# Kernel optimization log

Hardware: AMD Instinct MI355X
Metric: run time of the kernel (lower is better)

The kernel has to match this reference:

```python
import jax, jax.numpy as jnp
import numpy as np

N_EMBD = 768
N_HEAD = 12
HEAD_DIM = N_EMBD // N_HEAD
EPS = 1e-6


def setup_inputs() -> dict:
    key = jax.random.key(0)
    ks = jax.random.split(key, 8)
    B, T, C = 4, 2048, N_EMBD
    s = 0.02
    return {
        "x": jax.random.normal(ks[0], (B, T, C), jnp.float32),
        "ln1_w": jnp.ones((C,), jnp.float32),
        "ln1_b": jnp.zeros((C,), jnp.float32),
        "W_attn": jax.random.normal(ks[1], (C, 3 * C), jnp.float32) * s,
        "b_attn": jnp.zeros((3 * C,), jnp.float32),
        "W_attn_proj": jax.random.normal(ks[2], (C, C), jnp.float32) * s,
        "b_attn_proj": jnp.zeros((C,), jnp.float32),
        "ln2_w": jnp.ones((C,), jnp.float32),
        "ln2_b": jnp.zeros((C,), jnp.float32),
        "W_fc": jax.random.normal(ks[3], (C, 4 * C), jnp.float32) * s,
        "b_fc": jnp.zeros((4 * C,), jnp.float32),
        "W_mlp_proj": jax.random.normal(ks[4], (4 * C, C), jnp.float32) * s,
        "b_mlp_proj": jnp.zeros((C,), jnp.float32),
    }


def layer_norm(x, w, b):
    # Faithful to MyLayerNorm: (x - mean) / (std + eps), std with ddof=0
    mean = jnp.mean(x, axis=-1, keepdims=True)
    std = jnp.sqrt(jnp.mean((x - mean) ** 2, axis=-1, keepdims=True))
    return w * (x - mean) / (std + EPS) + b


def attention(h, W_attn, b_attn, W_proj, b_proj):
    B, T, C = h.shape
    qkv = h @ W_attn + b_attn                      # [B,T,3C]
    q, k, v = jnp.split(qkv, 3, axis=-1)
    # [B,T,C] -> [B,H,T,D]
    def to_heads(t):
        return t.reshape(B, T, N_HEAD, HEAD_DIM).transpose(0, 2, 1, 3)
    q, k, v = to_heads(q), to_heads(k), to_heads(v)
    att = jnp.einsum("bhtd,bhsd->bhts", q, k) * (1.0 / np.sqrt(HEAD_DIM))
    causal = jnp.tril(jnp.ones((T, T), bool))[None, None]
    att = jnp.where(causal, att, -jnp.inf)
    att = jax.nn.softmax(att, axis=-1)
    y = jnp.einsum("bhts,bhsd->bhtd", att, v)      # [B,H,T,D]
    y = y.transpose(0, 2, 1, 3).reshape(B, T, C)
    return y @ W_proj + b_proj


def mlp(h, W_fc, b_fc, W_proj, b_proj):
    h = jax.nn.gelu(h @ W_fc + b_fc, approximate=False)
    return h @ W_proj + b_proj


def reference(x, ln1_w, ln1_b, W_attn, b_attn, W_attn_proj, b_attn_proj,
              ln2_w, ln2_b, W_fc, b_fc, W_mlp_proj, b_mlp_proj):
    x = x + attention(layer_norm(x, ln1_w, ln1_b), W_attn, b_attn, W_attn_proj, b_attn_proj)
    x = x + mlp(layer_norm(x, ln2_w, ln2_b), W_fc, b_fc, W_mlp_proj, b_mlp_proj)
    return x
```

## Files before the change

### kernel.cpp

```cpp
#include <hip/hip_runtime.h>
#include <hip/hip_bf16.h>
#include <math.h>

#define N_EMBD 768
#define N_HEAD 12
#define HEAD_DIM 64
#define TOKENS 8192
#define SEQ 2048
#define BATCH 4
#define NQT (SEQ / 64)

typedef __attribute__((ext_vector_type(8))) short short8;
typedef __attribute__((ext_vector_type(4))) short short4v;
typedef __attribute__((ext_vector_type(4))) float f32x4;

__device__ __forceinline__ short f2bf(float f) {
    unsigned u = __builtin_bit_cast(unsigned, f);
    unsigned r = (u + 0x7fffu + ((u >> 16) & 1u)) >> 16;
    return (short)r;
}
__device__ __forceinline__ short f2bf_fast(float f) {
    unsigned u = __builtin_bit_cast(unsigned, f);
    return (short)((u + 0x8000u) >> 16);
}

__device__ __forceinline__ float exp2_raw(float x) {
#if __has_builtin(__builtin_amdgcn_exp2f)
    return __builtin_amdgcn_exp2f(x);
#else
    return exp2f(x);
#endif
}

__device__ __forceinline__ float gelu_fast(float x) {
    float z = 1.5957691216057308f * x * (1.0f + 0.044715f * x * x);
    return x / (1.0f + __expf(-z));
}

__device__ __forceinline__ void gld16(const void* g, void* l) {
    __builtin_amdgcn_global_load_lds(
        (const __attribute__((address_space(1))) unsigned int*)g,
        (__attribute__((address_space(3))) unsigned int*)l, 16, 0, 0);
}

__global__ __launch_bounds__(256) void wT_all(
        const float* __restrict__ Wa, short* __restrict__ Ta,
        const float* __restrict__ Wp, short* __restrict__ Tp,
        const float* __restrict__ Wf, short* __restrict__ Tf,
        const float* __restrict__ Wm, short* __restrict__ Tm) {
    __shared__ float T[32][33];
    int id = blockIdx.x;
    const float* W; short* Wt; int K, N;
    if (id < 1728)      { W = Wa; Wt = Ta; K = 768;  N = 2304; }
    else if (id < 2304) { W = Wp; Wt = Tp; K = 768;  N = 768;  id -= 1728; }
    else if (id < 4608) { W = Wf; Wt = Tf; K = 768;  N = 3072; id -= 2304; }
    else                { W = Wm; Wt = Tm; K = 3072; N = 768;  id -= 4608; }
    int tn = N >> 5;
    int n0 = (id % tn) * 32, k0 = (id / tn) * 32;
    int c = threadIdx.x & 31, r0 = threadIdx.x >> 5;
#pragma unroll
    for (int i = 0; i < 32; i += 8)
        T[r0 + i][c] = W[(size_t)(k0 + r0 + i) * N + n0 + c];
    __syncthreads();
#pragma unroll
    for (int i = 0; i < 32; i += 8)
        Wt[(size_t)(n0 + r0 + i) * K + k0 + c] = f2bf(T[c][r0 + i]);
}

__global__ __launch_bounds__(256) void ln_bf_kernel(const float* __restrict__ x,
                                                    const float* __restrict__ w,
                                                    const float* __restrict__ b,
                                                    short* __restrict__ out) {
    int row = blockIdx.x * 4 + (threadIdx.x >> 6);
    int lane = threadIdx.x & 63;
    const float4* xr = (const float4*)(x + (size_t)row * N_EMBD);
    const float4* wr = (const float4*)w;
    const float4* br = (const float4*)b;

    float4 v[3];
#pragma unroll
    for (int i = 0; i < 3; ++i) v[i] = xr[lane + 64 * i];
    float s = 0.f;
#pragma unroll
    for (int i = 0; i < 3; ++i) s += v[i].x + v[i].y + v[i].z + v[i].w;
#pragma unroll
    for (int off = 1; off < 64; off <<= 1) s += __shfl_xor(s, off, 64);
    float mean = s * (1.f / 768.f);

    float var = 0.f;
#pragma unroll
    for (int i = 0; i < 3; ++i) {
        float a0 = v[i].x - mean, a1 = v[i].y - mean,
              a2 = v[i].z - mean, a3 = v[i].w - mean;
        var += a0 * a0 + a1 * a1 + a2 * a2 + a3 * a3;
    }
#pragma unroll
    for (int off = 1; off < 64; off <<= 1) var += __shfl_xor(var, off, 64);
    float inv = 1.f / (sqrtf(var * (1.f / 768.f)) + 1e-6f);

    short4v* yr = (short4v*)(out + (size_t)row * N_EMBD);
#pragma unroll
    for (int i = 0; i < 3; ++i) {
        float4 wv = wr[lane + 64 * i], bv = br[lane + 64 * i];
        short4v o;
        o[0] = f2bf(wv.x * (v[i].x - mean) * inv + bv.x);
        o[1] = f2bf(wv.y * (v[i].y - mean) * inv + bv.y);
        o[2] = f2bf(wv.z * (v[i].z - mean) * inv + bv.z);
        o[3] = f2bf(wv.w * (v[i].w - mean) * inv + bv.w);
        yr[lane + 64 * i] = o;
    }
}

template <int ACT, int VOUT, int SWAP>
__global__ __launch_bounds__(256) void gemm_mfma(
        const short* __restrict__ A,
        const short* __restrict__ Bt,
        const float* __restrict__ bias,
        short* __restrict__ outp,
        short* __restrict__ vt,
        int M, int N, int K) {
    __shared__ short As[8192];
    __shared__ short Bs[8192];
    int tid = threadIdx.x;
    int wave = tid >> 6, lane = tid & 63;
    int quad = lane >> 4, l15 = lane & 15;
    int m0 = blockIdx.x * 128, n0 = blockIdx.y * 128;
    int wm = wave >> 1, wn = wave & 1;
    int sr = lane >> 2, sc = (lane & 3) * 8;

    f32x4 acc[4][4];
#pragma unroll
    for (int i = 0; i < 4; ++i)
#pragma unroll
        for (int j = 0; j < 4; ++j) acc[i][j] = (f32x4){0.f, 0.f, 0.f, 0.f};

    const short* ag = A + (size_t)(m0 + wave * 32 + sr) * K + sc;
    const short* bg = Bt + (size_t)(n0 + wave * 32 + sr) * K + sc;
    int woff = wave * 1024;

    gld16(ag, &As[woff]);
    gld16(ag + (size_t)16 * K, &As[woff + 512]);
    gld16(bg, &Bs[woff]);
    gld16(bg + (size_t)16 * K, &Bs[woff + 512]);

    int nk = K >> 5;
    for (int it = 0; it < nk; ++it) {
        int cb = (it & 1) * 4096;
        __syncthreads();
        if (it + 1 < nk) {
            int nb = ((it + 1) & 1) * 4096 + woff;
            int kn = (it + 1) << 5;
            gld16(ag + kn, &As[nb]);
            gld16(ag + kn + (size_t)16 * K, &As[nb + 512]);
            gld16(bg + kn, &Bs[nb]);
            gld16(bg + kn + (size_t)16 * K, &Bs[nb + 512]);
        }
        short8 af[4], bfr[4];
#pragma unroll
        for (int mt = 0; mt < 4; ++mt)
            af[mt] = *(const short8*)&As[cb + (wm * 64 + mt * 16 + l15) * 32 + quad * 8];
#pragma unroll
        for (int nt = 0; nt < 4; ++nt)
            bfr[nt] = *(const short8*)&Bs[cb + (wn * 64 + nt * 16 + l15) * 32 + quad * 8];
#pragma unroll
        for (int mt = 0; mt < 4; ++mt)
#pragma unroll
            for (int nt = 0; nt < 4; ++nt) {
                if (SWAP)
                    acc[mt][nt] = __builtin_amdgcn_mfma_f32_16x16x32_bf16(
                        bfr[nt], af[mt], acc[mt][nt], 0, 0, 0);
                else
                    acc[mt][nt] = __builtin_amdgcn_mfma_f32_16x16x32_bf16(
                        af[mt], bfr[nt], acc[mt][nt], 0, 0, 0);
            }
    }

    if (SWAP) {
#pragma unroll
        for (int nt = 0; nt < 4; ++nt) {
            int colb = n0 + wn * 64 + nt * 16 + quad * 4;
            f32x4 b4 = *(const f32x4*)&bias[colb];
#pragma unroll
            for (int mt = 0; mt < 4; ++mt) {
                int row = m0 + wm * 64 + mt * 16 + l15;
                short4v o4;
#pragma unroll
                for (int r = 0; r < 4; ++r) {
                    float v = acc[mt][nt][r] + b4[r];
                    if (ACT) v = gelu_fast(v);
                    o4[r] = f2bf(v);
                }
                *(short4v*)&outp[(size_t)row * N + colb] = o4;
            }
        }
        return;
    }

    if (VOUT && n0 >= 1536) {
#pragma unroll
        for (int mt = 0; mt < 4; ++mt) {
            int row0 = m0 + wm * 64 + mt * 16 + quad * 4;
            int b = row0 >> 11, t0 = row0 & 2047;
#pragma unroll
            for (int nt = 0; nt < 4; ++nt) {
                int col = n0 + wn * 64 + nt * 16 + l15;
                int vcol = col - 1536;
                int bh = b * N_HEAD + (vcol >> 6);
                int d = vcol & 63;
                float bi = bias[col];
                short4v o;
#pragma unroll
                for (int r = 0; r < 4; ++r) o[r] = f2bf(acc[mt][nt][r] + bi);
                *(short4v*)&vt[((size_t)bh * 64 + d) * SEQ + t0] = o;
            }
        }
        return;
    }

#pragma unroll
    for (int mt = 0; mt < 4; ++mt) {
        int row0 = m0 + wm * 64 + mt * 16 + quad * 4;
#pragma unroll
        for (int nt = 0; nt < 4; ++nt) {
            int col = n0 + wn * 64 + nt * 16 + l15;
            float bi = bias[col];
#pragma unroll
            for (int r = 0; r < 4; ++r) {
                float v = acc[mt][nt][r] + bi;
                if (ACT) v = gelu_fast(v);
                outp[(size_t)(row0 + r) * N + col] = f2bf(v);
            }
        }
    }
}

__global__ __launch_bounds__(256) void gemm_mfma_n64(
        const short* __restrict__ A,
        const short* __restrict__ Bt,
        const float* __restrict__ bias,
        const float* __restrict__ res,
        float* __restrict__ outp,
        int M, int N, int K) {
    __shared__ short As[16384];
    __shared__ short Bs[8192];
    int tid = threadIdx.x;
    int wave = tid >> 6, lane = tid & 63;
    int quad = lane >> 4, l15 = lane & 15;
    int m0 = blockIdx.x * 128, n0 = blockIdx.y * 64;
    int wm = wave >> 1, wn = wave & 1;
    int sr = lane >> 2, sc = (lane & 3) * 8;

    f32x4 acc[4][2];
#pragma unroll
    for (int i = 0; i < 4; ++i)
#pragma unroll
        for (int j = 0; j < 2; ++j) acc[i][j] = (f32x4){0.f, 0.f, 0.f, 0.f};

    const short* gptr[6];
    int loff[6];
    bool isa[6];
#pragma unroll
    for (int j = 0; j < 6; ++j) {
        int c = wave * 6 + j;
        if (c < 16) {
            int ks = c >> 3, r0 = (c & 7) * 16;
            gptr[j] = A + (size_t)(m0 + r0 + sr) * K + ks * 32 + sc;
            loff[j] = ks * 4096 + r0 * 32; isa[j] = true;
        } else {
            int cb = c - 16;
            int ks = cb >> 2, r0 = (cb & 3) * 16;
            gptr[j] = Bt + (size_t)(n0 + r0 + sr) * K + ks * 32 + sc;
            loff[j] = ks * 2048 + r0 * 32; isa[j] = false;
        }
    }
    int nk = K >> 6;

    auto stage = [&](int t) {
        int ba = (t & 1) << 13, bb = (t & 1) << 12;
        int kn = t << 6;
#pragma unroll
        for (int j = 0; j < 6; ++j)
            gld16(gptr[j] + kn, isa[j] ? &As[ba + loff[j]] : &Bs[bb + loff[j]]);
    };

    stage(0);

    for (int it = 0; it < nk; ++it) {
        int cba = (it & 1) << 13, cbb = (it & 1) << 12;
        __syncthreads();
        if (it + 1 < nk) stage(it + 1);
#pragma unroll
        for (int ks = 0; ks < 2; ++ks) {
            short8 af[4], bfr[2];
#pragma unroll
            for (int mt = 0; mt < 4; ++mt)
                af[mt] = *(const short8*)&As[cba + ks * 4096 +
                                             (wm * 64 + mt * 16 + l15) * 32 + quad * 8];
#pragma unroll
            for (int nt = 0; nt < 2; ++nt)
                bfr[nt] = *(const short8*)&Bs[cbb + ks * 2048 +
                                              (wn * 32 + nt * 16 + l15) * 32 + quad * 8];
#pragma unroll
            for (int mt = 0; mt < 4; ++mt)
#pragma unroll
                for (int nt = 0; nt < 2; ++nt)
                    acc[mt][nt] = __builtin_amdgcn_mfma_f32_16x16x32_bf16(
                        bfr[nt], af[mt], acc[mt][nt], 0, 0, 0);
        }
    }

#pragma unroll
    for (int nt = 0; nt < 2; ++nt) {
        int colb = n0 + wn * 32 + nt * 16 + quad * 4;
        f32x4 b4 = *(const f32x4*)&bias[colb];
#pragma unroll
        for (int mt = 0; mt < 4; ++mt) {
            int row = m0 + wm * 64 + mt * 16 + l15;
            f32x4 rv = *(const f32x4*)&res[(size_t)row * N + colb];
            f32x4 ov;
#pragma unroll
            for (int r = 0; r < 4; ++r) ov[r] = acc[mt][nt][r] + b4[r] + rv[r];
            *(f32x4*)&outp[(size_t)row * N + colb] = ov;
        }
    }
}

template <bool DIAG>
__device__ __forceinline__ void attn_kt(
        const short* __restrict__ Ks, const short* __restrict__ Vs,
        short* __restrict__ Ps, int cb,
        const short8* qf, short8 ones,
        f32x4* o, f32x4& lacc,
        int wave, int quad, int l15, int pswz) {
    f32x4 sacc[4];
#pragma unroll
    for (int nt = 0; nt < 4; ++nt) sacc[nt] = (f32x4){0.f, 0.f, 0.f, 0.f};
#pragma unroll
    for (int nt = 0; nt < 4; ++nt)
#pragma unroll
        for (int ks = 0; ks < 2; ++ks) {
            short8 kf = *(const short8*)&Ks[cb + ks * 2048 + (nt * 16 + l15) * 32 + quad * 8];
            sacc[nt] = __builtin_amdgcn_mfma_f32_16x16x32_bf16(qf[ks], kf, sacc[nt], 0, 0, 0);
        }

#pragma unroll
    for (int nt = 0; nt < 4; ++nt) {
        int scol = nt * 16 + l15;
        int base = (scol >> 5) * 2048 + (scol & 31);
#pragma unroll
        for (int r = 0; r < 4; ++r) {
            float p = exp2_raw(fmaf(sacc[nt][r], 0.18033688011112042f,
                                    -5.770780163555854f));
            if (DIAG && (scol > wave * 16 + quad * 4 + r)) p = 0.f;
            Ps[(base + (wave * 16 + quad * 4 + r) * 32) ^ (quad << 4)] = f2bf_fast(p);
        }
    }

    short8 pf0 = *(const short8*)&Ps[((wave * 16 + l15) * 32 + quad * 8) ^ pswz];
    short8 pf1 = *(const short8*)&Ps[(2048 + (wave * 16 + l15) * 32 + quad * 8) ^ pswz];
    lacc = __builtin_amdgcn_mfma_f32_16x16x32_bf16(pf0, ones, lacc, 0, 0, 0);
    lacc = __builtin_amdgcn_mfma_f32_16x16x32_bf16(pf1, ones, lacc, 0, 0, 0);
#pragma unroll
    for (int nt = 0; nt < 4; ++nt) {
        short8 vf0 = *(const short8*)&Vs[cb + (nt * 16 + l15) * 32 + quad * 8];
        short8 vf1 = *(const short8*)&Vs[cb + 2048 + (nt * 16 + l15) * 32 + quad * 8];
        o[nt] = __builtin_amdgcn_mfma_f32_16x16x32_bf16(pf0, vf0, o[nt], 0, 0, 0);
        o[nt] = __builtin_amdgcn_mfma_f32_16x16x32_bf16(pf1, vf1, o[nt], 0, 0, 0);
    }
}

__device__ __forceinline__ void attn_tile(
        const short* __restrict__ qkv, const short* __restrict__ Vt,
        short* __restrict__ y, int bh, int qt,
        short* Ks, short* Vs, short* Ps) {
    int tid = threadIdx.x;
    int wave = tid >> 6, lane = tid & 63;
    int quad = lane >> 4, l15 = lane & 15;
    int h = bh % N_HEAD, b = bh / N_HEAD;
    size_t bT = (size_t)b * SEQ;
    int q0 = qt * 64;
    int sr = lane >> 2, sc = (lane & 3) * 8;

    const short ONE_BF = (short)0x3F80;
    short8 ones;
#pragma unroll
    for (int j = 0; j < 8; ++j) ones[j] = ONE_BF;

    const short* qrow = qkv + (bT + q0 + wave * 16 + l15) * 2304 + h * 64 + quad * 8;
    short8 qf[2];
    qf[0] = *(const short8*)qrow;
    qf[1] = *(const short8*)(qrow + 32);

    const short* gp[4];
    int lo[4], adv[4];
#pragma unroll
    for (int j = 0; j < 4; ++j) {
        int c = wave * 4 + j;
        if (c < 8) {
            int sub = c >> 2, r0 = (c & 3) * 16;
            gp[j] = qkv + (bT + r0 + sr) * 2304 + 768 + h * 64 + sub * 32 + sc;
            lo[j] = sub * 2048 + r0 * 32;
            adv[j] = 64 * 2304;
        } else {
            int cv = c - 8;
            int sub = cv >> 2, r0 = (cv & 3) * 16;
            gp[j] = Vt + ((size_t)bh * 64 + r0 + sr) * SEQ + sub * 32 + sc;
            lo[j] = sub * 2048 + r0 * 32;
            adv[j] = 64;
        }
    }

    __syncthreads();
#pragma unroll
    for (int j = 0; j < 4; ++j)
        gld16(gp[j], (wave * 4 + j < 8) ? &Ks[lo[j]] : &Vs[lo[j]]);
#pragma unroll
    for (int j = 0; j < 4; ++j) gp[j] += adv[j];
    __syncthreads();

    f32x4 o[4];
#pragma unroll
    for (int nt = 0; nt < 4; ++nt) o[nt] = (f32x4){0.f, 0.f, 0.f, 0.f};
    f32x4 lacc = (f32x4){0.f, 0.f, 0.f, 0.f};

    const int pswz = ((l15 >> 2) & 3) << 4;

    for (int kt = 0; kt < qt; ++kt) {
        int cb = (kt & 1) * 4096;
        if (kt) __syncthreads();
        int nb = ((kt + 1) & 1) * 4096;
#pragma unroll
        for (int j = 0; j < 4; ++j) {
            gld16(gp[j], (wave * 4 + j < 8) ? &Ks[nb + lo[j]] : &Vs[nb + lo[j]]);
            gp[j] += adv[j];
        }
        attn_kt<false>(Ks, Vs, Ps, cb, qf, ones, o, lacc, wave, quad, l15, pswz);
    }

    if (qt) __syncthreads();
    attn_kt<true>(Ks, Vs, Ps, (qt & 1) * 4096, qf, ones, o, lacc,
                  wave, quad, l15, pswz);

    float inv[4];
#pragma unroll
    for (int r = 0; r < 4; ++r) inv[r] = 1.f / lacc[r];
#pragma unroll
    for (int nt = 0; nt < 4; ++nt)
#pragma unroll
        for (int r = 0; r < 4; ++r)
            y[(bT + q0 + wave * 16 + quad * 4 + r) * N_EMBD + h * 64 + nt * 16 + l15] =
                f2bf(o[nt][r] * inv[r]);
}

__global__ __launch_bounds__(256, 4) void attn_mfma(
        const short* __restrict__ qkv, const short* __restrict__ Vt,
        short* __restrict__ y) {
    __shared__ short Ks[8192], Vs[8192], Ps[4096];
    int bh = blockIdx.x;
    int pair = blockIdx.y;
    attn_tile(qkv, Vt, y, bh, pair, Ks, Vs, Ps);
    attn_tile(qkv, Vt, y, bh, NQT - 1 - pair, Ks, Vs, Ps);
}

extern "C" void kernel_launch(void* const* d_in, const int* in_sizes, int n_in,
                              void* d_out, int out_size, void* d_ws, size_t ws_size,
                              hipStream_t stream) {
    const float* x         = (const float*)d_in[0];
    const float* ln1_w     = (const float*)d_in[1];
    const float* ln1_b     = (const float*)d_in[2];
    const float* W_attn    = (const float*)d_in[3];
    const float* b_attn    = (const float*)d_in[4];
    const float* W_attn_pr = (const float*)d_in[5];
    const float* b_attn_pr = (const float*)d_in[6];
    const float* ln2_w     = (const float*)d_in[7];
    const float* ln2_b     = (const float*)d_in[8];
    const float* W_fc      = (const float*)d_in[9];
    const float* b_fc      = (const float*)d_in[10];
    const float* W_mlp_pr  = (const float*)d_in[11];
    const float* b_mlp_pr  = (const float*)d_in[12];
    float* out = (float*)d_out;

    const int M = TOKENS, C = N_EMBD;
    char* ws = (char*)d_ws;
    size_t region0 = (size_t)M * 3072 * 2;
    short* qkv_bf = (short*)ws;
    short* fc_bf  = (short*)ws;
    size_t off = region0;
    short* VtB   = (short*)(ws + off); off += (size_t)48 * 64 * SEQ * 2;
    short* yb    = (short*)(ws + off); off += (size_t)M * C * 2;
    short* lnb   = (short*)(ws + off); off += (size_t)M * C * 2;
    float* x1    = (float*)(ws + off); off += (size_t)M * C * 4;
    short* WaT   = (short*)(ws + off); off += (size_t)2304 * 768 * 2;
    short* WpT   = (short*)(ws + off); off += (size_t)768 * 768 * 2;
    short* WfT   = (short*)(ws + off); off += (size_t)3072 * 768 * 2;
    short* WmT   = (short*)(ws + off); off += (size_t)768 * 3072 * 2;

    wT_all<<<6912, 256, 0, stream>>>(W_attn, WaT, W_attn_pr, WpT,
                                     W_fc, WfT, W_mlp_pr, WmT);

    ln_bf_kernel<<<M / 4, 256, 0, stream>>>(x, ln1_w, ln1_b, lnb);

    gemm_mfma<0, 1, 0><<<dim3(M / 128, 2304 / 128), 256, 0, stream>>>(
        lnb, WaT, b_attn, qkv_bf, VtB, M, 2304, 768);

    attn_mfma<<<dim3(BATCH * N_HEAD, NQT / 2), 256, 0, stream>>>(qkv_bf, VtB, yb);

    gemm_mfma_n64<<<dim3(M / 128, 768 / 64), 256, 0, stream>>>(
        yb, WpT, b_attn_pr, x, x1, M, 768, 768);

    ln_bf_kernel<<<M / 4, 256, 0, stream>>>(x1, ln2_w, ln2_b, lnb);

    gemm_mfma<1, 0, 1><<<dim3(M / 128, 3072 / 128), 256, 0, stream>>>(
        lnb, WfT, b_fc, fc_bf, nullptr, M, 3072, 768);

    gemm_mfma_n64<<<dim3(M / 128, 768 / 64), 256, 0, stream>>>(
        fc_bf, WmT, b_mlp_pr, x1, out, M, 768, 3072);
}
```

Baseline: 371.5 us.

## Deepen GEMM K-tile to 64 and share K/V tiles across paired query tiles

The GEMM kernel now stages a 64-wide K slice per iteration, doubling shared memory per buffer, which halves the number of barriers and loop iterations. The attention kernel now processes its two paired query tiles (pair and NQT-1-pair) in a single pass over the key/value tiles, so the shared K/V tiles for the short tile are loaded once instead of twice. The cost is more registers for two sets of accumulators and more LDS in the GEMM (64KB), which may reduce occupancy.

```diff
diff --git a/kernel.cpp b/kernel.cpp
--- a/kernel.cpp
+++ b/kernel.cpp
@@ -119,8 +119,8 @@
         short* __restrict__ outp,
         short* __restrict__ vt,
         int M, int N, int K) {
-    __shared__ short As[8192];
-    __shared__ short Bs[8192];
+    __shared__ short As[16384];
+    __shared__ short Bs[16384];
     int tid = threadIdx.x;
     int wave = tid >> 6, lane = tid & 63;
     int quad = lane >> 4, l15 = lane & 15;
@@ -134,45 +134,61 @@
 #pragma unroll
         for (int j = 0; j < 4; ++j) acc[i][j] = (f32x4){0.f, 0.f, 0.f, 0.f};
 
-    const short* ag = A + (size_t)(m0 + wave * 32 + sr) * K + sc;
-    const short* bg = Bt + (size_t)(n0 + wave * 32 + sr) * K + sc;
-    int woff = wave * 1024;
-
-    gld16(ag, &As[woff]);
-    gld16(ag + (size_t)16 * K, &As[woff + 512]);
-    gld16(bg, &Bs[woff]);
-    gld16(bg + (size_t)16 * K, &Bs[woff + 512]);
-
-    int nk = K >> 5;
+    const short* gp[8];
+    int lo[8];
+    bool ia[8];
+#pragma unroll
+    for (int j = 0; j < 8; ++j) {
+        int c = wave * 8 + j;
+        if (c < 16) {
+            int ks = c >> 3, r0 = (c & 7) * 16;
+            gp[j] = A + (size_t)(m0 + r0 + sr) * K + ks * 32 + sc;
+            lo[j] = ks * 4096 + r0 * 32; ia[j] = true;
+        } else {
+            int cc = c - 16, ks = cc >> 3, r0 = (cc & 7) * 16;
+            gp[j] = Bt + (size_t)(n0 + r0 + sr) * K + ks * 32 + sc;
+            lo[j] = ks * 4096 + r0 * 32; ia[j] = false;
+        }
+    }
+    int nk = K >> 6;
+
+    auto stage = [&](int t) {
+        int bb = (t & 1) * 8192;
+        int kn = t << 6;
+#pragma unroll
+        for (int j = 0; j < 8; ++j)
+            gld16(gp[j] + kn, ia[j] ? &As[bb + lo[j]] : &Bs[bb + lo[j]]);
+    };
+
+    stage(0);
+
     for (int it = 0; it < nk; ++it) {
-        int cb = (it & 1) * 4096;
+        int cb = (it & 1) * 8192;
         __syncthreads();
-        if (it + 1 < nk) {
-            int nb = ((it + 1) & 1) * 4096 + woff;
-            int kn = (it + 1) << 5;
-            gld16(ag + kn, &As[nb]);
-            gld16(ag + kn + (size_t)16 * K, &As[nb + 512]);
-            gld16(bg + kn, &Bs[nb]);
-            gld16(bg + kn + (size_t)16 * K, &Bs[nb + 512]);
-        }
-        short8 af[4], bfr[4];
-#pragma unroll
-        for (int mt = 0; mt < 4; ++mt)
-            af[mt] = *(const short8*)&As[cb + (wm * 64 + mt * 16 + l15) * 32 + quad * 8];
-#pragma unroll
-        for (int nt = 0; nt < 4; ++nt)
-            bfr[nt] = *(const short8*)&Bs[cb + (wn * 64 + nt * 16 + l15) * 32 + quad * 8];
-#pragma unroll
-        for (int mt = 0; mt < 4; ++mt)
-#pragma unroll
-            for (int nt = 0; nt < 4; ++nt) {
-                if (SWAP)
-                    acc[mt][nt] = __builtin_amdgcn_mfma_f32_16x16x32_bf16(
-                        bfr[nt], af[mt], acc[mt][nt], 0, 0, 0);
-                else
-                    acc[mt][nt] = __builtin_amdgcn_mfma_f32_16x16x32_bf16(
-                        af[mt], bfr[nt], acc[mt][nt], 0, 0, 0);
-            }
+        if (it + 1 < nk) stage(it + 1);
+#pragma unroll
+        for (int ks = 0; ks < 2; ++ks) {
+            short8 af[4], bfr[4];
+#pragma unroll
+            for (int mt = 0; mt < 4; ++mt)
+                af[mt] = *(const short8*)&As[cb + ks * 4096 +
+                                             (wm * 64 + mt * 16 + l15) * 32 + quad * 8];
+#pragma unroll
+            for (int nt = 0; nt < 4; ++nt)
+                bfr[nt] = *(const short8*)&Bs[cb + ks * 4096 +
+                                              (wn * 64 + nt * 16 + l15) * 32 + quad * 8];
+#pragma unroll
+            for (int mt = 0; mt < 4; ++mt)
+#pragma unroll
+                for (int nt = 0; nt < 4; ++nt) {
+                    if (SWAP)
+                        acc[mt][nt] = __builtin_amdgcn_mfma_f32_16x16x32_bf16(
+                            bfr[nt], af[mt], acc[mt][nt], 0, 0, 0);
+                    else
+                        acc[mt][nt] = __builtin_amdgcn_mfma_f32_16x16x32_bf16(
+                            af[mt], bfr[nt], acc[mt][nt], 0, 0, 0);
+                }
+        }
     }
 
     if (SWAP) {
@@ -369,16 +385,15 @@
     }
 }
 
-__device__ __forceinline__ void attn_tile(
+__device__ __forceinline__ void attn_pair(
         const short* __restrict__ qkv, const short* __restrict__ Vt,
-        short* __restrict__ y, int bh, int qt,
+        short* __restrict__ y, int bh, int qta, int qtb,
         short* Ks, short* Vs, short* Ps) {
     int tid = threadIdx.x;
     int wave = tid >> 6, lane = tid & 63;
     int quad = lane >> 4, l15 = lane & 15;
     int h = bh % N_HEAD, b = bh / N_HEAD;
     size_t bT = (size_t)b * SEQ;
-    int q0 = qt * 64;
     int sr = lane >> 2, sc = (lane & 3) * 8;
 
     const short ONE_BF = (short)0x3F80;
@@ -386,10 +401,11 @@
 #pragma unroll
     for (int j = 0; j < 8; ++j) ones[j] = ONE_BF;
 
-    const short* qrow = qkv + (bT + q0 + wave * 16 + l15) * 2304 + h * 64 + quad * 8;
-    short8 qf[2];
-    qf[0] = *(const short8*)qrow;
-    qf[1] = *(const short8*)(qrow + 32);
+    const short* qrowA = qkv + (bT + qta * 64 + wave * 16 + l15) * 2304 + h * 64 + quad * 8;
+    const short* qrowB = qkv + (bT + qtb * 64 + wave * 16 + l15) * 2304 + h * 64 + quad * 8;
+    short8 qfA[2], qfB[2];
+    qfA[0] = *(const short8*)qrowA; qfA[1] = *(const short8*)(qrowA + 32);
+    qfB[0] = *(const short8*)qrowB; qfB[1] = *(const short8*)(qrowB + 32);
 
     const short* gp[4];
     int lo[4], adv[4];
@@ -410,22 +426,25 @@
         }
     }
 
+#pragma unroll
+    for (int j = 0; j < 4; ++j) {
+        gld16(gp[j], (wave * 4 + j < 8) ? &Ks[lo[j]] : &Vs[lo[j]]);
+        gp[j] += adv[j];
+    }
     __syncthreads();
-#pragma unroll
-    for (int j = 0; j < 4; ++j)
-        gld16(gp[j], (wave * 4 + j < 8) ? &Ks[lo[j]] : &Vs[lo[j]]);
-#pragma unroll
-    for (int j = 0; j < 4; ++j) gp[j] += adv[j];
-    __syncthreads();
-
-    f32x4 o[4];
-#pragma unroll
-    for (int nt = 0; nt < 4; ++nt) o[nt] = (f32x4){0.f, 0.f, 0.f, 0.f};
-    f32x4 lacc = (f32x4){0.f, 0.f, 0.f, 0.f};
+
+    f32x4 oA[4], oB[4];
+#pragma unroll
+    for (int nt = 0; nt < 4; ++nt) {
+        oA[nt] = (f32x4){0.f, 0.f, 0.f, 0.f};
+        oB[nt] = (f32x4){0.f, 0.f, 0.f, 0.f};
+    }
+    f32x4 laccA = (f32x4){0.f, 0.f, 0.f, 0.f};
+    f32x4 laccB = (f32x4){0.f, 0.f, 0.f, 0.f};
 
     const int pswz = ((l15 >> 2) & 3) << 4;
 
-    for (int kt = 0; kt < qt; ++kt) {
+    for (int kt = 0; kt < qtb; ++kt) {
         int cb = (kt & 1) * 4096;
         if (kt) __syncthreads();
         int nb = ((kt + 1) & 1) * 4096;
@@ -434,32 +453,37 @@
             gld16(gp[j], (wave * 4 + j < 8) ? &Ks[nb + lo[j]] : &Vs[nb + lo[j]]);
             gp[j] += adv[j];
         }
-        attn_kt<false>(Ks, Vs, Ps, cb, qf, ones, o, lacc, wave, quad, l15, pswz);
-    }
-
-    if (qt) __syncthreads();
-    attn_kt<true>(Ks, Vs, Ps, (qt & 1) * 4096, qf, ones, o, lacc,
+        if (kt < qta)
+            attn_kt<false>(Ks, Vs, Ps, cb, qfA, ones, oA, laccA, wave, quad, l15, pswz);
+        else if (kt == qta)
+            attn_kt<true>(Ks, Vs, Ps, cb, qfA, ones, oA, laccA, wave, quad, l15, pswz);
+        attn_kt<false>(Ks, Vs, Ps, cb, qfB, ones, oB, laccB, wave, quad, l15, pswz);
+    }
+
+    __syncthreads();
+    attn_kt<true>(Ks, Vs, Ps, (qtb & 1) * 4096, qfB, ones, oB, laccB,
                   wave, quad, l15, pswz);
 
-    float inv[4];
-#pragma unroll
-    for (int r = 0; r < 4; ++r) inv[r] = 1.f / lacc[r];
+    float invA[4], invB[4];
+#pragma unroll
+    for (int r = 0; r < 4; ++r) { invA[r] = 1.f / laccA[r]; invB[r] = 1.f / laccB[r]; }
 #pragma unroll
     for (int nt = 0; nt < 4; ++nt)
 #pragma unroll
-        for (int r = 0; r < 4; ++r)
-            y[(bT + q0 + wave * 16 + quad * 4 + r) * N_EMBD + h * 64 + nt * 16 + l15] =
-                f2bf(o[nt][r] * inv[r]);
+        for (int r = 0; r < 4; ++r) {
+            y[(bT + qta * 64 + wave * 16 + quad * 4 + r) * N_EMBD + h * 64 + nt * 16 + l15] =
+                f2bf(oA[nt][r] * invA[r]);
+            y[(bT + qtb * 64 + wave * 16 + quad * 4 + r) * N_EMBD + h * 64 + nt * 16 + l15] =
+                f2bf(oB[nt][r] * invB[r]);
+        }
 }
 
 __global__ __launch_bounds__(256, 4) void attn_mfma(
         const short* __restrict__ qkv, const short* __restrict__ Vt,
         short* __restrict__ y) {
     __shared__ short Ks[8192], Vs[8192], Ps[4096];
-    int bh = blockIdx.x;
     int pair = blockIdx.y;
-    attn_tile(qkv, Vt, y, bh, pair, Ks, Vs, Ps);
-    attn_tile(qkv, Vt, y, bh, NQT - 1 - pair, Ks, Vs, Ps);
+    attn_pair(qkv, Vt, y, blockIdx.x, pair, NQT - 1 - pair, Ks, Vs, Ps);
 }
 
 extern "C" void kernel_launch(void* const* d_in, const int* in_sizes, int n_in,
```

Measured after the change: 350.3 us. 1.06x faster.
